# Performance work log

Hardware: AMD Instinct MI355X
Metric: run time of the kernel (lower is better)

The kernel has to match this reference:

```python
import jax, jax.numpy as jnp
import numpy as np

# Dimensions (see shape_source)
B, D, Q, M = 2, 1024, 1024, 1024
K = Q + M                      # klen = mlen + qlen
N_HEAD, D_HEAD = 16, 64        # n_head * d_head == d_model
D_INNER = 4096
LOCAL_SIZE = 1000              # Attention: self.local_size or 1000
EPS = 1e-5                     # F.layer_norm default eps


def setup_inputs() -> dict:
    key = jax.random.key(0)
    ks = jax.random.split(key, 12)
    z = jax.random.normal(ks[0], (B, D, Q), jnp.float32)
    z_hist = jax.random.normal(ks[1], (B, D, M), jnp.float32)
    u = jax.random.normal(ks[2], (B, 3 * N_HEAD * D_HEAD, K), jnp.float32) * 0.1
    # sinusoidal relative position embedding (PositionalEmbedding), positions K-1..0
    inv_freq = 1.0 / (10000.0 ** (jnp.arange(0, D, 2, dtype=jnp.float32) / D))
    pos_seq = jnp.arange(K - 1, -1, -1, dtype=jnp.float32)
    sinusoid = inv_freq[:, None] * pos_seq[None, :]  # (D/2, K)
    pos_emb = jnp.concatenate([jnp.sin(sinusoid), jnp.cos(sinusoid)], axis=0)[None]  # (1, D, K)
    s = 0.02
    W_qkv = jax.random.normal(ks[3], (3 * N_HEAD * D_HEAD, D), jnp.float32) * s
    W_r = jax.random.normal(ks[4], (N_HEAD * D_HEAD, D), jnp.float32) * s
    r_w_bias = jax.random.uniform(ks[5], (N_HEAD, D_HEAD), jnp.float32, -0.05, 0.05)
    r_r_bias = jax.random.uniform(ks[6], (N_HEAD, D_HEAD), jnp.float32, -0.05, 0.05)
    W_o = jax.random.normal(ks[7], (D, N_HEAD * D_HEAD), jnp.float32) * s
    b_o = jnp.zeros((D,), jnp.float32)
    W_ff1 = jax.random.normal(ks[8], (D_INNER, D), jnp.float32) * s
    b_ff1 = jnp.zeros((D_INNER,), jnp.float32)
    W_ff2 = jax.random.normal(ks[9], (D, D_INNER), jnp.float32) * s
    b_ff2 = jnp.zeros((D,), jnp.float32)
    return dict(z=z, z_hist=z_hist, u=u, pos_emb=pos_emb, W_qkv=W_qkv, W_r=W_r,
                r_w_bias=r_w_bias, r_r_bias=r_r_bias, W_o=W_o, b_o=b_o,
                W_ff1=W_ff1, b_ff1=b_ff1, W_ff2=W_ff2, b_ff2=b_ff2)


def _ln(x, axis):
    # F.layer_norm without affine params
    mu = jnp.mean(x, axis=axis, keepdims=True)
    var = jnp.var(x, axis=axis, keepdims=True)
    return (x - mu) / jnp.sqrt(var + EPS)


def _rel_shift(x):
    # Transformer-XL relative shift: pad left on key dim, reinterpret, drop row.
    b, n, q, k = x.shape
    x = jnp.pad(x, ((0, 0), (0, 0), (0, 0), (1, 0)))
    x = x.reshape(b, n, k + 1, q)
    return x[:, :, 1:, :].reshape(b, n, q, k)


def reference(z, z_hist, u, pos_emb, W_qkv, W_r, r_w_bias, r_r_bias, W_o, b_o,
              W_ff1, b_ff1, W_ff2, b_ff2):
    scale = 1.0 / (D_HEAD ** 0.5)
    # ---- Attention (post-LN, Conv1d kernel=1 == pointwise matmul) ----
    cat = jnp.concatenate([z_hist, z], axis=2)                 # (B, D, K)
    w_heads = jnp.einsum('od,bdk->bok', W_qkv, cat) + u        # (B, 3*n*dh, K)
    q_h, k_h, v_h = jnp.split(w_heads, 3, axis=1)
    q_h = q_h[:, :, -Q:].reshape(B, N_HEAD, D_HEAD, Q)
    k_h = k_h.reshape(B, N_HEAD, D_HEAD, K)
    v_h = v_h.reshape(B, N_HEAD, D_HEAD, K)
    r_k = jnp.einsum('od,dk->ok', W_r, pos_emb[0]).reshape(N_HEAD, D_HEAD, K)
    AC = jnp.einsum('bndi,bndj->bnij', q_h + r_w_bias[:, :, None], k_h)
    BD = _rel_shift(jnp.einsum('bndi,ndj->bnij', q_h + r_r_bias[:, :, None], r_k))
    score = (AC + BD) * scale                                  # (B, n, Q, K)
    causal = jnp.triu(jnp.ones((Q, K), bool), k=1 + M)         # future tokens
    local = jnp.tril(jnp.ones((Q, K), bool), k=M - LOCAL_SIZE)  # beyond local window
    mask = causal | local
    score = jnp.where(mask[None, None], -jnp.inf, score)
    prob = jax.nn.softmax(score, axis=-1)
    attn_vec = jnp.einsum('bnij,bndj->bndi', prob, v_h).reshape(B, N_HEAD * D_HEAD, Q)
    attn_out = jnp.einsum('od,bdq->boq', W_o, attn_vec) + b_o[None, :, None]
    out = _ln(attn_out + z, axis=1)                            # LN over d_model (dim=1)
    # ---- FFN (operates token-major) ----
    h = out.transpose(0, 2, 1)                                 # (B, Q, D)
    ff = jnp.maximum(h @ W_ff1.T + b_ff1, 0.0) @ W_ff2.T + b_ff2
    y = _ln(ff + h, axis=-1)
    return y.transpose(0, 2, 1)                                # (B, D, Q)
```

## Files before the change

### kernel.cpp

```cpp
#include <hip/hip_runtime.h>

#define D_MODEL 1024
#define QLEN 1024

typedef __bf16 bf16x8 __attribute__((ext_vector_type(8)));
typedef __bf16 bf16x4 __attribute__((ext_vector_type(4)));
typedef float f32x4 __attribute__((ext_vector_type(4)));

__device__ __forceinline__ void gload16(const void* g, void* l) {
    __builtin_amdgcn_global_load_lds(
        (const __attribute__((address_space(1))) void*)g,
        (__attribute__((address_space(3))) void*)l, 16, 0, 0);
}

__device__ __forceinline__ void gemm_core8(
    __bf16* __restrict__ smA, __bf16* __restrict__ smB,
    const __bf16* __restrict__ A, const __bf16* __restrict__ Bt,
    float* __restrict__ C, __bf16* __restrict__ Cb,
    const float* __restrict__ U, const float* __restrict__ Ut,
    const float* __restrict__ bias,
    int K, int lda, int ldb, int ldC, int ldU, int relu, int m0, int n0)
{
    const int t = threadIdx.x;
    const int lane = t & 63, w = t >> 6;
    const int l15 = lane & 15, lg = lane >> 4;
    const int wm = w >> 2, wn = w & 3;
    const int srow = lane >> 3, cpr = lane & 7;
    const int NK = K >> 6;
    const int SZ = 128 * 64;

    #define STAGE(buf, kt)                                                                   \
    {                                                                                        \
        int k0s = (kt) * 64;                                                                 \
        _Pragma("unroll")                                                                    \
        for (int i = 0; i < 2; ++i) {                                                        \
            int r = w * 16 + i * 8 + srow;                                                   \
            int c = cpr ^ (r & 7);                                                           \
            gload16(&A[(long long)(m0 + r) * lda + k0s + c * 8],                             \
                    &smA[(buf) * SZ + (w * 16 + i * 8) * 64]);                               \
            gload16(&Bt[(long long)(n0 + r) * ldb + k0s + c * 8],                            \
                    &smB[(buf) * SZ + (w * 16 + i * 8) * 64]);                               \
        }                                                                                    \
    }

    f32x4 acc[4][2] = {};
    STAGE(0, 0);

    for (int kt = 0; kt < NK; ++kt) {
        const int cb = kt & 1;
        if (kt + 1 < NK) {
            STAGE(cb ^ 1, kt + 1);
            asm volatile("s_waitcnt vmcnt(4)" ::: "memory");
        } else {
            asm volatile("s_waitcnt vmcnt(0)" ::: "memory");
        }
        __builtin_amdgcn_sched_barrier(0);
        __builtin_amdgcn_s_barrier();

        #pragma unroll
        for (int kk = 0; kk < 2; ++kk) {
            bf16x8 bfr[2];
            #pragma unroll
            for (int nt = 0; nt < 2; ++nt) {
                int nr = wn * 32 + nt * 16 + l15;
                bfr[nt] = *(const bf16x8*)&smB[cb * SZ + nr * 64 + (((kk * 4 + lg) ^ (nr & 7)) * 8)];
            }
            #pragma unroll
            for (int mt = 0; mt < 4; ++mt) {
                int mr = wm * 64 + mt * 16 + l15;
                bf16x8 afr = *(const bf16x8*)&smA[cb * SZ + mr * 64 + (((kk * 4 + lg) ^ (mr & 7)) * 8)];
                #pragma unroll
                for (int nt = 0; nt < 2; ++nt)
                    acc[mt][nt] = __builtin_amdgcn_mfma_f32_16x16x32_bf16(afr, bfr[nt], acc[mt][nt], 0, 0, 0);
            }
        }
        asm volatile("s_waitcnt lgkmcnt(0)" ::: "memory");
        __builtin_amdgcn_sched_barrier(0);
        __builtin_amdgcn_s_barrier();
    }
    #undef STAGE

    if (Ut) {
        float* uf = (float*)smA;
        #pragma unroll
        for (int hh = 0; hh < 2; ++hh) {
            __syncthreads();
            int r = t >> 3, c0 = (t & 7) * 16;
            const float* src = &Ut[(long long)(n0 + hh * 64 + r) * ldU + m0 + c0];
            #pragma unroll
            for (int k = 0; k < 4; ++k)
                *(float4*)&uf[r * 132 + c0 + k * 4] = *(const float4*)&src[k * 4];
            __syncthreads();
            if ((wn >> 1) == hh) {
                #pragma unroll
                for (int nt = 0; nt < 2; ++nt) {
                    int rr = wn * 32 + nt * 16 + l15 - hh * 64;
                    #pragma unroll
                    for (int mt = 0; mt < 4; ++mt) {
                        #pragma unroll
                        for (int rg = 0; rg < 4; ++rg) {
                            int m = wm * 64 + mt * 16 + lg * 4 + rg;
                            acc[mt][nt][rg] += uf[rr * 132 + m];
                        }
                    }
                }
            }
        }
    }

    #pragma unroll
    for (int mt = 0; mt < 4; ++mt) {
        #pragma unroll
        for (int nt = 0; nt < 2; ++nt) {
            #pragma unroll
            for (int rg = 0; rg < 4; ++rg) {
                int m = m0 + wm * 64 + mt * 16 + lg * 4 + rg;
                int n = n0 + wn * 32 + nt * 16 + l15;
                float v = acc[mt][nt][rg];
                if (U)    v += U[(long long)m * ldU + n];
                if (bias) v += bias[n];
                if (relu) v = fmaxf(v, 0.0f);
                if (Cb) Cb[(long long)m * ldC + n] = (__bf16)v;
                else    C [(long long)m * ldC + n] = v;
            }
        }
    }
}

template<int KSPLIT>
__global__ __launch_bounds__(512) void gemm_bf16_k(
    const __bf16* __restrict__ A, const __bf16* __restrict__ Bt,
    float* __restrict__ C0, float* __restrict__ C1,
    __bf16* __restrict__ Cb,
    const float* __restrict__ U, const float* __restrict__ bias,
    int K, int lda, int ldb, int ldC, int ldU, int relu)
{
    __shared__ __bf16 SM[32768];
    int yb = blockIdx.y;
    int half = 0;
    if (KSPLIT > 1) { half = yb & (KSPLIT - 1); yb /= KSPLIT; }
    const int Keff = K / KSPLIT;
    A  += (long long)half * Keff;
    Bt += (long long)half * Keff;
    float* C = half ? C1 : C0;
    if (half) { bias = nullptr; U = nullptr; }
    gemm_core8(SM, SM + 16384, A, Bt, C, Cb, U, nullptr, bias,
               Keff, lda, ldb, ldC, ldU, relu, yb * 128, blockIdx.x * 128);
}

__global__ __launch_bounds__(512) void gemm_fused3(
    const __bf16* __restrict__ cat_t, const __bf16* __restrict__ Wqkvb,
    __bf16* __restrict__ qkT, const float* __restrict__ u,
    __bf16* __restrict__ wh_v,
    const __bf16* __restrict__ pos_t, const __bf16* __restrict__ Wrb,
    __bf16* __restrict__ rkT)
{
    __shared__ __bf16 SM[32768];
    int bid = blockIdx.x;
    if (bid < 512) {
        int zz = bid >> 8, rem = bid & 255, y = rem >> 4, x = rem & 15;
        gemm_core8(SM, SM + 16384,
                   cat_t + (long long)zz * 2097152, Wqkvb,
                   nullptr, qkT + (long long)zz * 4194304,
                   nullptr, u + (long long)zz * 6291456, nullptr,
                   1024, 1024, 1024, 2048, 2048, 0, y * 128, x * 128);
    } else if (bid < 768) {
        int l = bid - 512, zz = l >> 7, rem = l & 127, y = rem >> 4, x = rem & 15;
        gemm_core8(SM, SM + 16384,
                   Wqkvb + 2048 * 1024, cat_t + (long long)zz * 2097152,
                   nullptr, wh_v + (long long)zz * 2097152,
                   u + 4194304 + (long long)zz * 6291456, nullptr, nullptr,
                   1024, 1024, 1024, 2048, 2048, 0, y * 128, x * 128);
    } else {
        int l = bid - 768, y = l >> 3, x = l & 7;
        gemm_core8(SM, SM + 16384,
                   pos_t + 960 * 1024, Wrb,
                   nullptr, rkT, nullptr, nullptr, nullptr,
                   1024, 1024, 1024, 1024, 0, 0, y * 128, x * 128);
    }
}

__global__ __launch_bounds__(256) void prep_all(
    const float* __restrict__ Wqkv, __bf16* __restrict__ Wqkvb,
    const float* __restrict__ Wr,   __bf16* __restrict__ Wrb,
    const float* __restrict__ Wo,   __bf16* __restrict__ Wob,
    const float* __restrict__ Wff1, __bf16* __restrict__ Wff1b,
    const float* __restrict__ Wff2, __bf16* __restrict__ Wff2b,
    const float* __restrict__ zh, const float* __restrict__ z, __bf16* __restrict__ cat_t,
    const float* __restrict__ pos, __bf16* __restrict__ pos_t)
{
    __shared__ float ts[32][33];
    int bid = blockIdx.x;
    const int t = threadIdx.x;
    if (bid < 13312) {
        long long i = ((long long)bid * 256 + t) * 4;
        const float* s; __bf16* dd;
        if (i < 3145728)                    { s = Wqkv + i; dd = Wqkvb + i; }
        else if ((i -= 3145728) < 1048576)  { s = Wr + i;   dd = Wrb + i; }
        else if ((i -= 1048576) < 1048576)  { s = Wo + i;   dd = Wob + i; }
        else if ((i -= 1048576) < 4194304)  { s = Wff1 + i; dd = Wff1b + i; }
        else { i -= 4194304;                  s = Wff2 + i; dd = Wff2b + i; }
        float4 v = *(const float4*)s;
        bf16x4 o = { (__bf16)v.x, (__bf16)v.y, (__bf16)v.z, (__bf16)v.w };
        *(bf16x4*)dd = o;
        return;
    }
    bid -= 13312;
    const float* S; __bf16* D; int R, Cc, bx, by;
    if (bid < 2048) {
        int zz = bid >> 10, r2 = bid & 1023;
        S = zh + (long long)zz * 1048576; D = cat_t + (long long)zz * 2097152;
        R = 1024; Cc = 1024; bx = r2 & 31; by = r2 >> 5;
    } else if (bid < 4096) {
        int l = bid - 2048; int zz = l >> 10, r2 = l & 1023;
        S = z + (long long)zz * 1048576; D = cat_t + 1048576 + (long long)zz * 2097152;
        R = 1024; Cc = 1024; bx = r2 & 31; by = r2 >> 5;
    } else if (bid < 6144) {
        int l = bid - 4096;
        S = pos; D = pos_t; R = 1024; Cc = 2048; bx = l & 63; by = l >> 6;
    } else {
        int l = bid - 6144;
        int i = (l * 256 + t) * 4;
        bf16x4 zv = { (__bf16)0.f, (__bf16)0.f, (__bf16)0.f, (__bf16)0.f };
        *(bf16x4*)&pos_t[2048 * 1024 + i] = zv;
        return;
    }
    int r0 = by * 32, c0 = bx * 32;
    int tr = t >> 5, tc = t & 31;
    #pragma unroll
    for (int p = 0; p < 4; ++p)
        ts[tr + p * 8][tc] = S[(long long)(r0 + tr + p * 8) * Cc + c0 + tc];
    __syncthreads();
    #pragma unroll
    for (int p = 0; p < 4; ++p)
        D[(long long)(c0 + tr + p * 8) * R + r0 + tc] = (__bf16)ts[tc][tr + p * 8];
}

__global__ __launch_bounds__(256) void attn_mfma(
    const __bf16* __restrict__ QKT, const __bf16* __restrict__ WHV,
    const __bf16* __restrict__ RKT,
    const float* __restrict__ rwb, const float* __restrict__ rrb,
    __bf16* __restrict__ AVt)
{
    __shared__ __bf16 SM[38144];
    __bf16* KT0 = SM;
    __bf16* KT1 = SM + 4096;
    __bf16* VS0 = SM + 8192;
    __bf16* VS1 = SM + 12288;
    __bf16* RT  = SM + 16384;
    __bf16* PS  = SM + 28672;
    __bf16* BT  = SM + 32768;

    const int d = blockIdx.x;
    const int xcd = d & 7, idx = d >> 3;
    const int qt = idx & 15;
    const int gq = xcd + 8 * (idx >> 4);
    const int b = gq >> 4, n = gq & 15;
    const int i0 = qt * 64;

    const int t = threadIdx.x;
    const int lane = t & 63, w = t >> 6;
    const int l15 = lane & 15, lg = lane >> 4;
    const int fco = n * 64;

    const __bf16* qkb = QKT + (long long)b * (2048 * 2048);
    const __bf16* vb  = WHV + (long long)b * (1024 * 2048) + (long long)fco * 2048;
    __bf16* BTw = BT + w * 1344;

    #pragma unroll
    for (int pp = 0; pp < 2; ++pp) {
        int cid = pp * 256 + t;
        int q = cid >> 3, s = cid & 7, c = s ^ (q & 7);
        bf16x8 qv = *(const bf16x8*)&qkb[(long long)(1024 + i0 + q) * 2048 + fco + c * 8];
        bf16x8 ow, orr;
        #pragma unroll
        for (int e = 0; e < 8; ++e) {
            float qf = (float)qv[e];
            ow[e]  = (__bf16)(qf + rwb[fco + c * 8 + e]);
            orr[e] = (__bf16)(qf + rrb[fco + c * 8 + e]);
        }
        *(bf16x8*)&PS[q * 64 + s * 8] = ow;
        *(bf16x8*)&VS0[q * 64 + s * 8] = orr;
    }
    __syncthreads();

    #define LDF(buf, row, ch) (*(const bf16x8*)&(buf)[(row) * 64 + ((((ch) ^ ((row) & 7))) * 8)])

    const int mrow = w * 16 + l15;
    bf16x8 qw0 = LDF(PS, mrow, lg), qw1 = LDF(PS, mrow, lg + 4);
    bf16x8 qr0 = LDF(VS0, mrow, lg), qr1 = LDF(VS0, mrow, lg + 4);
    asm volatile("s_waitcnt lgkmcnt(0)" ::: "memory");
    __builtin_amdgcn_sched_barrier(0);
    __builtin_amdgcn_s_barrier();

    #pragma unroll
    for (int pp = 0; pp < 2; ++pp) {
        int cid = pp * 256 + t;
        int r = cid >> 3, s = cid & 7, c = s ^ (r & 7);
        gload16(&qkb[(long long)(i0 + r) * 2048 + 1024 + fco + c * 8], &KT0[(pp * 32 + w * 8) * 64]);
        gload16(&vb[(long long)r * 2048 + i0 + c * 8], &VS0[(pp * 32 + w * 8) * 64]);
    }
    #pragma unroll
    for (int pp = 0; pp < 6; ++pp) {
        int cid = pp * 256 + t;
        int r = cid >> 3, s = cid & 7, c = s ^ (r & 7);
        gload16(&RKT[(long long)r * 1024 + fco + c * 8], &RT[(pp * 32 + w * 8) * 64]);
    }
    asm volatile("s_waitcnt vmcnt(0)" ::: "memory");
    __builtin_amdgcn_sched_barrier(0);
    __builtin_amdgcn_s_barrier();

    const bf16x8 ones = { (__bf16)1.f, (__bf16)1.f, (__bf16)1.f, (__bf16)1.f,
                          (__bf16)1.f, (__bf16)1.f, (__bf16)1.f, (__bf16)1.f };

    f32x4 O0 = {}, O1 = {}, O2 = {}, O3 = {};
    float rm[4] = {-1e30f, -1e30f, -1e30f, -1e30f};
    float rl[4] = {0.f, 0.f, 0.f, 0.f};
    int cur = 0;

    for (int kt = 0; kt <= 16; ++kt) {
        __bf16* KTc = cur ? KT1 : KT0;
        __bf16* VSc = cur ? VS1 : VS0;
        __bf16* KTn = cur ? KT0 : KT1;
        __bf16* VSn = cur ? VS0 : VS1;
        const int rbase = (kt % 3) * 64;

        if (kt < 16) {
            int j0n = i0 + (kt + 1) * 64;
            #pragma unroll
            for (int pp = 0; pp < 2; ++pp) {
                int cid = pp * 256 + t;
                int r = cid >> 3, s = cid & 7, c = s ^ (r & 7);
                gload16(&qkb[(long long)(j0n + r) * 2048 + 1024 + fco + c * 8], &KTn[(pp * 32 + w * 8) * 64]);
                gload16(&vb[(long long)r * 2048 + j0n + c * 8], &VSn[(pp * 32 + w * 8) * 64]);
            }
            int rb = kt * 64 + 128;
            int lb = ((kt + 2) % 3) * 64;
            #pragma unroll
            for (int pp = 0; pp < 2; ++pp) {
                int cid = pp * 256 + t;
                int r = cid >> 3, s = cid & 7, c = s ^ (r & 7);
                gload16(&RKT[(long long)(rb + r) * 1024 + fco + c * 8], &RT[(lb + pp * 32 + w * 8) * 64]);
            }
        }
        __builtin_amdgcn_sched_barrier(0);

        __builtin_amdgcn_s_setprio(1);
        #pragma unroll
        for (int k5 = 0; k5 < 5; ++k5) {
            int pr = (3 - w + k5) * 16 + l15;
            int lr = rbase + pr; if (lr >= 192) lr -= 192;
            const __bf16* rrow = &RT[lr * 64];
            f32x4 cc = {};
            cc = __builtin_amdgcn_mfma_f32_16x16x32_bf16(qr0, *(const bf16x8*)&rrow[((lg ^ (pr & 7)) * 8)], cc, 0, 0, 0);
            cc = __builtin_amdgcn_mfma_f32_16x16x32_bf16(qr1, *(const bf16x8*)&rrow[(((lg + 4) ^ (pr & 7)) * 8)], cc, 0, 0, 0);
            #pragma unroll
            for (int rg = 0; rg < 4; ++rg)
                BTw[(lg * 4 + rg) * 84 + k5 * 16 + l15] = (__bf16)cc[rg];
        }
        __builtin_amdgcn_s_setprio(0);

        f32x4 cc4[4];
        __builtin_amdgcn_s_setprio(1);
        #pragma unroll
        for (int nt = 0; nt < 4; ++nt) {
            int jr = nt * 16 + l15;
            f32x4 cc = {};
            cc = __builtin_amdgcn_mfma_f32_16x16x32_bf16(qw0, LDF(KTc, jr, lg), cc, 0, 0, 0);
            cc = __builtin_amdgcn_mfma_f32_16x16x32_bf16(qw1, LDF(KTc, jr, lg + 4), cc, 0, 0, 0);
            cc4[nt] = cc;
        }
        __builtin_amdgcn_s_setprio(0);

        const bool bnd = (kt < 2) | (kt == 16);
        float sv[4][4];
        if (!bnd) {
            #pragma unroll
            for (int nt = 0; nt < 4; ++nt) {
                int jr = nt * 16 + l15;
                #pragma unroll
                for (int rg = 0; rg < 4; ++rg) {
                    int r4 = lg * 4 + rg;
                    sv[nt][rg] = (cc4[nt][rg] + (float)BTw[r4 * 84 + jr - r4 + 15]) * 0.125f;
                }
            }
        } else {
            #pragma unroll
            for (int nt = 0; nt < 4; ++nt) {
                int jr = nt * 16 + l15;
                #pragma unroll
                for (int rg = 0; rg < 4; ++rg) {
                    int r4 = lg * 4 + rg;
                    int dji = jr - (w * 16 + r4);
                    float s = (cc4[nt][rg] + (float)BTw[r4 * 84 + jr - r4 + 15]) * 0.125f;
                    bool valid = (kt == 0) ? (dji >= 25)
                               : (kt == 1) ? (dji >= -39)
                               : (dji <= 0);
                    sv[nt][rg] = valid ? s : -1e30f;
                }
            }
        }

        float lmax[4];
        bool need = false;
        #pragma unroll
        for (int rg = 0; rg < 4; ++rg) {
            lmax[rg] = fmaxf(fmaxf(sv[0][rg], sv[1][rg]), fmaxf(sv[2][rg], sv[3][rg]));
            need = need || (lmax[rg] > rm[rg] + 8.0f);
        }
        if (__any(need)) {
            #pragma unroll
            for (int rg = 0; rg < 4; ++rg) {
                float m = lmax[rg];
                m = fmaxf(m, __shfl_xor(m, 1, 16));
                m = fmaxf(m, __shfl_xor(m, 2, 16));
                m = fmaxf(m, __shfl_xor(m, 4, 16));
                m = fmaxf(m, __shfl_xor(m, 8, 16));
                float nm = fmaxf(rm[rg], m);
                float fac = __expf(rm[rg] - nm);
                rm[rg] = nm;
                rl[rg] *= fac;
                O0[rg] *= fac; O1[rg] *= fac; O2[rg] *= fac; O3[rg] *= fac;
            }
        }

        if (!bnd) {
            #pragma unroll
            for (int nt = 0; nt < 4; ++nt) {
                int jc = nt * 16 + l15;
                #pragma unroll
                for (int rg = 0; rg < 4; ++rg) {
                    float p = __expf(sv[nt][rg] - rm[rg]);
                    int row = w * 16 + lg * 4 + rg;
                    PS[row * 64 + (((jc >> 3) ^ (row & 7)) * 8) + (jc & 7)] = (__bf16)p;
                }
            }
        } else {
            #pragma unroll
            for (int nt = 0; nt < 4; ++nt) {
                int jc = nt * 16 + l15;
                #pragma unroll
                for (int rg = 0; rg < 4; ++rg) {
                    float p = (sv[nt][rg] > -1e29f) ? __expf(sv[nt][rg] - rm[rg]) : 0.0f;
                    int row = w * 16 + lg * 4 + rg;
                    PS[row * 64 + (((jc >> 3) ^ (row & 7)) * 8) + (jc & 7)] = (__bf16)p;
                }
            }
        }

        bf16x8 pa0 = LDF(PS, mrow, lg), pa1 = LDF(PS, mrow, lg + 4);
        f32x4 Os = {};
        __builtin_amdgcn_s_setprio(1);
        Os = __builtin_amdgcn_mfma_f32_16x16x32_bf16(pa0, ones, Os, 0, 0, 0);
        Os = __builtin_amdgcn_mfma_f32_16x16x32_bf16(pa1, ones, Os, 0, 0, 0);
        O0 = __builtin_amdgcn_mfma_f32_16x16x32_bf16(pa0, LDF(VSc,  0 + l15, lg),     O0, 0, 0, 0);
        O0 = __builtin_amdgcn_mfma_f32_16x16x32_bf16(pa1, LDF(VSc,  0 + l15, lg + 4), O0, 0, 0, 0);
        O1 = __builtin_amdgcn_mfma_f32_16x16x32_bf16(pa0, LDF(VSc, 16 + l15, lg),     O1, 0, 0, 0);
        O1 = __builtin_amdgcn_mfma_f32_16x16x32_bf16(pa1, LDF(VSc, 16 + l15, lg + 4), O1, 0, 0, 0);
        O2 = __builtin_amdgcn_mfma_f32_16x16x32_bf16(pa0, LDF(VSc, 32 + l15, lg),     O2, 0, 0, 0);
        O2 = __builtin_amdgcn_mfma_f32_16x16x32_bf16(pa1, LDF(VSc, 32 + l15, lg + 4), O2, 0, 0, 0);
        O3 = __builtin_amdgcn_mfma_f32_16x16x32_bf16(pa0, LDF(VSc, 48 + l15, lg),     O3, 0, 0, 0);
        O3 = __builtin_amdgcn_mfma_f32_16x16x32_bf16(pa1, LDF(VSc, 48 + l15, lg + 4), O3, 0, 0, 0);
        __builtin_amdgcn_s_setprio(0);
        #pragma unroll
        for (int rg = 0; rg < 4; ++rg) rl[rg] += Os[rg];

        asm volatile("s_waitcnt vmcnt(0)" ::: "memory");
        __builtin_amdgcn_sched_barrier(0);
        __builtin_amdgcn_s_barrier();
        cur ^= 1;
    }

    #pragma unroll
    for (int rg = 0; rg < 4; ++rg) {
        float inv = 1.0f / rl[rg];
        int q = i0 + w * 16 + lg * 4 + rg;
        long long base = ((long long)b * 1024 + q) * 1024 + fco;
        AVt[base +  0 + l15] = (__bf16)(O0[rg] * inv);
        AVt[base + 16 + l15] = (__bf16)(O1[rg] * inv);
        AVt[base + 32 + l15] = (__bf16)(O2[rg] * inv);
        AVt[base + 48 + l15] = (__bf16)(O3[rg] * inv);
    }
    #undef LDF
}

__global__ __launch_bounds__(256) void ln1_kernel(
    const float* __restrict__ A0, const float* __restrict__ A1,
    const float* __restrict__ bo, const __bf16* __restrict__ CatT,
    __bf16* __restrict__ Hb)
{
    int i = blockIdx.x, b = blockIdx.y, t = threadIdx.x;
    __shared__ float xs[D_MODEL];
    __shared__ float red[256];
    __shared__ float smu, srstd;
    long long tb = ((long long)b * 1024 + i) * 1024;
    long long zb = ((long long)b * 2048 + 1024 + i) * 1024;

    float lsum = 0.0f;
    for (int dd = t; dd < D_MODEL; dd += 256) {
        float v = A0[tb + dd] + A1[tb + dd] + bo[dd] + (float)CatT[zb + dd];
        xs[dd] = v;
        lsum += v;
    }
    red[t] = lsum; __syncthreads();
    for (int s2 = 128; s2 > 0; s2 >>= 1) { if (t < s2) red[t] += red[t + s2]; __syncthreads(); }
    if (t == 0) smu = red[0] * (1.0f / D_MODEL);
    __syncthreads();
    float mu = smu;

    float lq = 0.0f;
    for (int dd = t; dd < D_MODEL; dd += 256) { float c = xs[dd] - mu; lq += c * c; }
    red[t] = lq; __syncthreads();
    for (int s2 = 128; s2 > 0; s2 >>= 1) { if (t < s2) red[t] += red[t + s2]; __syncthreads(); }
    if (t == 0) srstd = rsqrtf(red[0] * (1.0f / D_MODEL) + 1e-5f);
    __syncthreads();
    float rstd = srstd;

    for (int dd = t; dd < D_MODEL; dd += 256)
        Hb[tb + dd] = (__bf16)((xs[dd] - mu) * rstd);
}

__global__ __launch_bounds__(256) void ln2_stats(
    const float* __restrict__ F0, const float* __restrict__ F1,
    const __bf16* __restrict__ Hb, float2* __restrict__ st)
{
    int i = blockIdx.x, b = blockIdx.y, t = threadIdx.x;
    __shared__ float rs[256], rq[256];
    long long tb = ((long long)b * 1024 + i) * 1024;

    float s = 0.f, q = 0.f;
    for (int dd = t; dd < D_MODEL; dd += 256) {
        float v = F0[tb + dd] + F1[tb + dd] + (float)Hb[tb + dd];
        s += v; q += v * v;
    }
    rs[t] = s; rq[t] = q; __syncthreads();
    for (int s2 = 128; s2 > 0; s2 >>= 1) {
        if (t < s2) { rs[t] += rs[t + s2]; rq[t] += rq[t + s2]; }
        __syncthreads();
    }
    if (t == 0) {
        float mu = rs[0] * (1.0f / D_MODEL);
        float var = rq[0] * (1.0f / D_MODEL) - mu * mu;
        st[(long long)b * 1024 + i] = make_float2(mu, rsqrtf(var + 1e-5f));
    }
}

__global__ __launch_bounds__(256) void ln2_write(
    const float* __restrict__ F0, const float* __restrict__ F1,
    const __bf16* __restrict__ Hb, const float2* __restrict__ st,
    float* __restrict__ OUT)
{
    __shared__ float ts[32][33];
    int f0 = blockIdx.x * 32, i0 = blockIdx.y * 32, b = blockIdx.z;
    int tr = threadIdx.x >> 5, tc = threadIdx.x & 31;
    #pragma unroll
    for (int p = 0; p < 4; ++p) {
        int tok = i0 + tr + p * 8;
        long long tb = ((long long)b * 1024 + tok) * 1024;
        float2 s = st[(long long)b * 1024 + tok];
        float v = F0[tb + f0 + tc] + F1[tb + f0 + tc] + (float)Hb[tb + f0 + tc];
        ts[tr + p * 8][tc] = (v - s.x) * s.y;
    }
    __syncthreads();
    #pragma unroll
    for (int p = 0; p < 4; ++p)
        OUT[((long long)b * 1024 + f0 + tr + p * 8) * 1024 + i0 + tc] = ts[tc][tr + p * 8];
}

extern "C" void kernel_launch(void* const* d_in, const int* in_sizes, int n_in,
                              void* d_out, int out_size, void* d_ws, size_t ws_size,
                              hipStream_t stream) {
    const float* z    = (const float*)d_in[0];
    const float* zh   = (const float*)d_in[1];
    const float* u    = (const float*)d_in[2];
    const float* pos  = (const float*)d_in[3];
    const float* Wqkv = (const float*)d_in[4];
    const float* Wr   = (const float*)d_in[5];
    const float* rwb  = (const float*)d_in[6];
    const float* rrb  = (const float*)d_in[7];
    const float* Wo   = (const float*)d_in[8];
    const float* bo   = (const float*)d_in[9];
    const float* Wff1 = (const float*)d_in[10];
    const float* bff1 = (const float*)d_in[11];
    const float* Wff2 = (const float*)d_in[12];
    const float* bff2 = (const float*)d_in[13];
    float* out = (float*)d_out;
    float* ws  = (float*)d_ws;

    __bf16* cat_t = (__bf16*)ws;
    __bf16* pos_t = (__bf16*)(ws + 2097152);
    __bf16* Wqkvb = (__bf16*)(ws + 3178496);
    __bf16* Wrb   = (__bf16*)(ws + 4751360);
    __bf16* Wob   = (__bf16*)(ws + 5275648);
    __bf16* Wff1b = (__bf16*)(ws + 5799936);
    __bf16* Wff2b = (__bf16*)(ws + 7897088);
    __bf16* qkT   = (__bf16*)(ws + 14188544);
    __bf16* wh_v  = (__bf16*)(ws + 18382848);
    __bf16* rkT   = (__bf16*)(ws + 20480000);
    __bf16* av_t  = (__bf16*)(ws + 21069824);
    float*  ao0   = ws + 22118400;
    float*  ao1   = ws + 24215552;
    __bf16* h_bf  = (__bf16*)(ws + 26312704);
    float2* st2   = (float2*)(ws + 27361280);
    __bf16* f1b   = (__bf16*)(ws + 14188544);
    float*  f20   = ws + 9994240;
    float*  f21   = ws + 12091392;

    prep_all<<<19520, 256, 0, stream>>>(
        Wqkv, Wqkvb, Wr, Wrb, Wo, Wob, Wff1, Wff1b, Wff2, Wff2b,
        zh, z, cat_t, pos, pos_t);

    gemm_fused3<<<840, 512, 0, stream>>>(
        cat_t, Wqkvb, qkT, u, wh_v, pos_t, Wrb, rkT);

    attn_mfma<<<512, 256, 0, stream>>>(qkT, wh_v, rkT, rwb, rrb, av_t);

    gemm_bf16_k<2><<<dim3(8, 32, 1), 512, 0, stream>>>(
        av_t, Wob, ao0, ao1, nullptr, nullptr, nullptr,
        1024, 1024, 1024, 1024, 0, 0);
    ln1_kernel<<<dim3(1024, 2), 256, 0, stream>>>(ao0, ao1, bo, cat_t, h_bf);
    gemm_bf16_k<1><<<dim3(32, 16, 1), 512, 0, stream>>>(
        h_bf, Wff1b, nullptr, nullptr, f1b, nullptr, bff1,
        1024, 1024, 1024, 4096, 0, 1);
    gemm_bf16_k<2><<<dim3(8, 32, 1), 512, 0, stream>>>(
        f1b, Wff2b, f20, f21, nullptr, nullptr, bff2,
        4096, 4096, 4096, 1024, 0, 0);
    ln2_stats<<<dim3(1024, 2), 256, 0, stream>>>(f20, f21, h_bf, st2);
    ln2_write<<<dim3(32, 32, 2), 256, 0, stream>>>(f20, f21, h_bf, st2, out);
}
```

Measured before the change: 207.1 us.

## Process 128 query rows per attention block with two wave groups sharing K/V tiles

The attention kernel moves from 64-query blocks of 4 waves to 128-query blocks of 8 waves. The two wave groups stagger by one key tile, so K, V and relative-position tiles loaded into shared memory serve twice as many queries, and the positional ring buffer grows from 3 to 4 slots. This halves global traffic for K/V/R per query. In exchange the grid shrinks to 256 blocks, there is one extra loop iteration of partially idle work, and LDS use per block rises.

```diff
diff --git a/kernel.cpp b/kernel.cpp
--- a/kernel.cpp
+++ b/kernel.cpp
@@ -236,31 +236,32 @@
         D[(long long)(c0 + tr + p * 8) * R + r0 + tc] = (__bf16)ts[tc][tr + p * 8];
 }
 
-__global__ __launch_bounds__(256) void attn_mfma(
+__global__ __launch_bounds__(512) void attn_mfma(
     const __bf16* __restrict__ QKT, const __bf16* __restrict__ WHV,
     const __bf16* __restrict__ RKT,
     const float* __restrict__ rwb, const float* __restrict__ rrb,
     __bf16* __restrict__ AVt)
 {
-    __shared__ __bf16 SM[38144];
+    __shared__ __bf16 SM[51712];
     __bf16* KT0 = SM;
     __bf16* KT1 = SM + 4096;
     __bf16* VS0 = SM + 8192;
     __bf16* VS1 = SM + 12288;
     __bf16* RT  = SM + 16384;
-    __bf16* PS  = SM + 28672;
-    __bf16* BT  = SM + 32768;
+    __bf16* PS  = SM + 32768;
+    __bf16* BT  = SM + 40960;
 
     const int d = blockIdx.x;
     const int xcd = d & 7, idx = d >> 3;
-    const int qt = idx & 15;
-    const int gq = xcd + 8 * (idx >> 4);
+    const int qt = idx & 7;
+    const int gq = xcd + 8 * (idx >> 3);
     const int b = gq >> 4, n = gq & 15;
-    const int i0 = qt * 64;
+    const int i0 = qt * 128;
 
     const int t = threadIdx.x;
     const int lane = t & 63, w = t >> 6;
     const int l15 = lane & 15, lg = lane >> 4;
+    const int g = w >> 2, wg = w & 3;
     const int fco = n * 64;
 
     const __bf16* qkb = QKT + (long long)b * (2048 * 2048);
@@ -269,7 +270,7 @@
 
     #pragma unroll
     for (int pp = 0; pp < 2; ++pp) {
-        int cid = pp * 256 + t;
+        int cid = pp * 512 + t;
         int q = cid >> 3, s = cid & 7, c = s ^ (q & 7);
         bf16x8 qv = *(const bf16x8*)&qkb[(long long)(1024 + i0 + q) * 2048 + fco + c * 8];
         bf16x8 ow, orr;
@@ -280,7 +281,7 @@
             orr[e] = (__bf16)(qf + rrb[fco + c * 8 + e]);
         }
         *(bf16x8*)&PS[q * 64 + s * 8] = ow;
-        *(bf16x8*)&VS0[q * 64 + s * 8] = orr;
+        *(bf16x8*)&RT[q * 64 + s * 8] = orr;
     }
     __syncthreads();
 
@@ -288,23 +289,21 @@
 
     const int mrow = w * 16 + l15;
     bf16x8 qw0 = LDF(PS, mrow, lg), qw1 = LDF(PS, mrow, lg + 4);
-    bf16x8 qr0 = LDF(VS0, mrow, lg), qr1 = LDF(VS0, mrow, lg + 4);
+    bf16x8 qr0 = LDF(RT, mrow, lg), qr1 = LDF(RT, mrow, lg + 4);
     asm volatile("s_waitcnt lgkmcnt(0)" ::: "memory");
     __builtin_amdgcn_sched_barrier(0);
     __builtin_amdgcn_s_barrier();
 
-    #pragma unroll
-    for (int pp = 0; pp < 2; ++pp) {
-        int cid = pp * 256 + t;
-        int r = cid >> 3, s = cid & 7, c = s ^ (r & 7);
-        gload16(&qkb[(long long)(i0 + r) * 2048 + 1024 + fco + c * 8], &KT0[(pp * 32 + w * 8) * 64]);
-        gload16(&vb[(long long)r * 2048 + i0 + c * 8], &VS0[(pp * 32 + w * 8) * 64]);
-    }
-    #pragma unroll
-    for (int pp = 0; pp < 6; ++pp) {
-        int cid = pp * 256 + t;
-        int r = cid >> 3, s = cid & 7, c = s ^ (r & 7);
-        gload16(&RKT[(long long)r * 1024 + fco + c * 8], &RT[(pp * 32 + w * 8) * 64]);
+    {
+        int r = t >> 3, s = t & 7, c = s ^ (r & 7);
+        gload16(&qkb[(long long)(i0 + r) * 2048 + 1024 + fco + c * 8], &KT0[(w * 8) * 64]);
+        gload16(&vb[(long long)r * 2048 + i0 + c * 8], &VS0[(w * 8) * 64]);
+        #pragma unroll
+        for (int pp = 0; pp < 3; ++pp) {
+            int cid = pp * 512 + t;
+            int rr = cid >> 3, ss = cid & 7, cc = ss ^ (rr & 7);
+            gload16(&RKT[(long long)rr * 1024 + fco + cc * 8], &RT[(pp * 64 + w * 8) * 64]);
+        }
     }
     asm volatile("s_waitcnt vmcnt(0)" ::: "memory");
     __builtin_amdgcn_sched_barrier(0);
@@ -318,38 +317,32 @@
     float rl[4] = {0.f, 0.f, 0.f, 0.f};
     int cur = 0;
 
-    for (int kt = 0; kt <= 16; ++kt) {
+    for (int kt = 0; kt <= 17; ++kt) {
         __bf16* KTc = cur ? KT1 : KT0;
         __bf16* VSc = cur ? VS1 : VS0;
         __bf16* KTn = cur ? KT0 : KT1;
         __bf16* VSn = cur ? VS0 : VS1;
-        const int rbase = (kt % 3) * 64;
-
+        const int ktr = kt - g;
+
+        if (kt < 17) {
+            int j0n = i0 + (kt + 1) * 64;
+            int r = t >> 3, s = t & 7, c = s ^ (r & 7);
+            gload16(&qkb[(long long)(j0n + r) * 2048 + 1024 + fco + c * 8], &KTn[(w * 8) * 64]);
+            gload16(&vb[(long long)r * 2048 + j0n + c * 8], &VSn[(w * 8) * 64]);
+        }
         if (kt < 16) {
-            int j0n = i0 + (kt + 1) * 64;
-            #pragma unroll
-            for (int pp = 0; pp < 2; ++pp) {
-                int cid = pp * 256 + t;
-                int r = cid >> 3, s = cid & 7, c = s ^ (r & 7);
-                gload16(&qkb[(long long)(j0n + r) * 2048 + 1024 + fco + c * 8], &KTn[(pp * 32 + w * 8) * 64]);
-                gload16(&vb[(long long)r * 2048 + j0n + c * 8], &VSn[(pp * 32 + w * 8) * 64]);
-            }
             int rb = kt * 64 + 128;
-            int lb = ((kt + 2) % 3) * 64;
-            #pragma unroll
-            for (int pp = 0; pp < 2; ++pp) {
-                int cid = pp * 256 + t;
-                int r = cid >> 3, s = cid & 7, c = s ^ (r & 7);
-                gload16(&RKT[(long long)(rb + r) * 1024 + fco + c * 8], &RT[(lb + pp * 32 + w * 8) * 64]);
-            }
+            int lb = ((kt + 2) & 3) * 64;
+            int r = t >> 3, s = t & 7, c = s ^ (r & 7);
+            gload16(&RKT[(long long)(rb + r) * 1024 + fco + c * 8], &RT[(lb + w * 8) * 64]);
         }
         __builtin_amdgcn_sched_barrier(0);
 
         __builtin_amdgcn_s_setprio(1);
         #pragma unroll
         for (int k5 = 0; k5 < 5; ++k5) {
-            int pr = (3 - w + k5) * 16 + l15;
-            int lr = rbase + pr; if (lr >= 192) lr -= 192;
+            int pr = (3 - wg + k5) * 16 + l15;
+            int lr = ((ktr * 64) + pr) & 255;
             const __bf16* rrow = &RT[lr * 64];
             f32x4 cc = {};
             cc = __builtin_amdgcn_mfma_f32_16x16x32_bf16(qr0, *(const bf16x8*)&rrow[((lg ^ (pr & 7)) * 8)], cc, 0, 0, 0);
@@ -372,7 +365,7 @@
         }
         __builtin_amdgcn_s_setprio(0);
 
-        const bool bnd = (kt < 2) | (kt == 16);
+        const bool bnd = (ktr <= 1) | (ktr >= 16);
         float sv[4][4];
         if (!bnd) {
             #pragma unroll
@@ -391,11 +384,11 @@
                 #pragma unroll
                 for (int rg = 0; rg < 4; ++rg) {
                     int r4 = lg * 4 + rg;
-                    int dji = jr - (w * 16 + r4);
+                    int dji = jr - (wg * 16 + r4);
                     float s = (cc4[nt][rg] + (float)BTw[r4 * 84 + jr - r4 + 15]) * 0.125f;
-                    bool valid = (kt == 0) ? (dji >= 25)
-                               : (kt == 1) ? (dji >= -39)
-                               : (dji <= 0);
+                    bool valid = (ktr == 0) ? (dji >= 25)
+                               : (ktr == 1) ? (dji >= -39)
+                               : (ktr == 16) ? (dji <= 0) : false;
                     sv[nt][rg] = valid ? s : -1e30f;
                 }
             }
@@ -613,7 +606,7 @@
     gemm_fused3<<<840, 512, 0, stream>>>(
         cat_t, Wqkvb, qkT, u, wh_v, pos_t, Wrb, rkT);
 
-    attn_mfma<<<512, 256, 0, stream>>>(qkT, wh_v, rkT, rwb, rrb, av_t);
+    attn_mfma<<<256, 512, 0, stream>>>(qkT, wh_v, rkT, rwb, rrb, av_t);
 
     gemm_bf16_k<2><<<dim3(8, 32, 1), 512, 0, stream>>>(
         av_t, Wob, ao0, ao1, nullptr, nullptr, nullptr,
```

Result: no change. 204.1 us (median of 2 runs) (-1.4%).
